# Kernel optimization log

Hardware: AMD Instinct MI355X
Metric: run time of the kernel (lower is better)

## Reference

```python
import jax, jax.numpy as jnp
import numpy as np

SCORE_THRESHOLD = 0.5
IOU_THRESHOLD = 0.5


def _pairwise_iou(boxes):
    # boxes: [N, 4] in xyxy
    x1, y1, x2, y2 = boxes[:, 0], boxes[:, 1], boxes[:, 2], boxes[:, 3]
    area = (x2 - x1) * (y2 - y1)  # [N]
    ix1 = jnp.maximum(x1[:, None], x1[None, :])
    iy1 = jnp.maximum(y1[:, None], y1[None, :])
    ix2 = jnp.minimum(x2[:, None], x2[None, :])
    iy2 = jnp.minimum(y2[:, None], y2[None, :])
    iw = jnp.clip(ix2 - ix1, 0.0)
    ih = jnp.clip(iy2 - iy1, 0.0)
    inter = iw * ih  # [N, N]
    union = area[:, None] + area[None, :] - inter
    return inter / jnp.maximum(union, 1e-9)


def setup_inputs() -> dict:
    key = jax.random.key(0)
    rtdetr_raw_out = jax.random.uniform(key, (1, 8192, 5), dtype=jnp.float32)
    return {"rtdetr_raw_out": rtdetr_raw_out}


def reference(rtdetr_raw_out):
    x = rtdetr_raw_out[0]                      # [N, 5]
    cxcywh = x[:, :4]
    conf = x[:, 4]
    conf = conf / jnp.max(conf)                # normalize by max score
    cx, cy, w, h = cxcywh[:, 0], cxcywh[:, 1], cxcywh[:, 2], cxcywh[:, 3]
    xyxy = jnp.stack([cx - w * 0.5, cy - h * 0.5, cx + w * 0.5, cy + h * 0.5], axis=1)
    valid = conf >= SCORE_THRESHOLD            # score filter
    N = xyxy.shape[0]
    # sort by descending score (torchvision nms processes boxes in score order)
    order = jnp.argsort(-conf)
    boxes_s = xyxy[order]
    scores_s = conf[order]
    valid_s = valid[order]
    iou = _pairwise_iou(boxes_s)               # [N, N]
    idx = jnp.arange(N)

    def body(i, keep):
        # if box i survives, suppress all lower-score boxes with IoU > thr
        sup = keep[i] & (iou[i] > IOU_THRESHOLD) & (idx > i)
        return keep & ~sup

    keep = jax.lax.fori_loop(0, N, body, valid_s)
    out = jnp.concatenate([boxes_s, scores_s[:, None]], axis=1)  # [N, 5]
    # fixed-shape output: suppressed / below-threshold rows are zeroed
    return jnp.where(keep[:, None], out, 0.0)
```

## Files before the change

### kernel.cpp

```cpp
#include <hip/hip_runtime.h>
#include <cstdint>

typedef unsigned long long ull;

#define N_BOX 8192
#define N_WORDS 128
#define CH 512
#define WPC 8
#define NBLK 16

#define OFF_TB     0
#define OFF_TC     3440640
#define OFF_TD     3932160
#define OFF_BOXES  4456448
#define OFF_SCORES 4587520
#define OFF_CTRL   4620288
#define OFF_KEPT   4624384

#define CTRL_VB   512
#define KSTRIDE   16

__device__ __forceinline__ int rows_before2(int c) {
    return 7424 * c - 256 * c * c;
}

__device__ __forceinline__ ull make_key(float s, int idx) {
    return (((ull)__float_as_uint(s)) << 13) | (ull)(8191 - idx);
}

__device__ __forceinline__ float box_area(float4 b) {
    return __fmul_rn(__fsub_rn(b.z, b.x), __fsub_rn(b.w, b.y));
}

__device__ __forceinline__ bool iou_gt_half(float4 a, float aarea, float4 b, float barea) {
    float ix1 = fmaxf(a.x, b.x);
    float iy1 = fmaxf(a.y, b.y);
    float ix2 = fminf(a.z, b.z);
    float iy2 = fminf(a.w, b.w);
    float iw = fmaxf(__fsub_rn(ix2, ix1), 0.0f);
    float ih = fmaxf(__fsub_rn(iy2, iy1), 0.0f);
    float inter = __fmul_rn(iw, ih);
    float uni = __fsub_rn(__fadd_rn(aarea, barea), inter);
    float iou = __fdiv_rn(inter, fmaxf(uni, 1e-9f));
    return iou > 0.5f;
}

__global__ __launch_bounds__(256) void k123_rank_scatter(const float* __restrict__ in,
                                                         float4* __restrict__ boxes4,
                                                         float* __restrict__ scores,
                                                         int* __restrict__ ctrl) {
    __shared__ ull keys[N_BOX];
    __shared__ float wm[4];
    __shared__ int wv[4];
    int t = threadIdx.x;
    int bx = blockIdx.x;

    float cf[32];
    float m = 0.0f;
    #pragma unroll
    for (int r = 0; r < 32; ++r) {
        cf[r] = in[(r * 256 + t) * 5 + 4];
        m = fmaxf(m, cf[r]);
    }
    for (int off = 32; off; off >>= 1) m = fmaxf(m, __shfl_down(m, off));
    if ((t & 63) == 0) wm[t >> 6] = m;
    __syncthreads();
    float maxc = fmaxf(fmaxf(wm[0], wm[1]), fmaxf(wm[2], wm[3]));

    #pragma unroll
    for (int r = 0; r < 32; ++r) {
        int k = r * 256 + t;
        keys[k] = make_key(__fdiv_rn(cf[r], maxc), k);
    }
    __syncthreads();

    int il = t >> 3, seg = t & 7;
    int i = bx * 32 + il;
    ull ki = keys[i];
    const ull* kb = keys + seg;
    int cnt = 0;
    #pragma unroll 8
    for (int cc = 0; cc < 1024; ++cc)
        cnt += (kb[cc * 8] > ki) ? 1 : 0;
    cnt += __shfl_down(cnt, 4, 8);
    cnt += __shfl_down(cnt, 2, 8);
    cnt += __shfl_down(cnt, 1, 8);

    if (seg == 0) {
        int r = cnt;
        float cx = in[i * 5 + 0];
        float cy = in[i * 5 + 1];
        float w  = in[i * 5 + 2];
        float h  = in[i * 5 + 3];
        float s  = __fdiv_rn(in[i * 5 + 4], maxc);
        float4 b;
        b.x = __fsub_rn(cx, __fmul_rn(w, 0.5f));
        b.y = __fsub_rn(cy, __fmul_rn(h, 0.5f));
        b.z = __fadd_rn(cx, __fmul_rn(w, 0.5f));
        b.w = __fadd_rn(cy, __fmul_rn(h, 0.5f));
        boxes4[r] = b;
        scores[r] = s;
    }

    if (bx == 0) {
        const ull kthr = ((ull)0x3F000000u) << 13;
        int cv = 0;
        for (int k = t; k < N_BOX; k += 256) cv += (keys[k] >= kthr) ? 1 : 0;
        for (int off = 32; off; off >>= 1) cv += __shfl_down(cv, off);
        if ((t & 63) == 0) wv[t >> 6] = cv;
        if (t < NBLK) ctrl[t * 32] = 0;
        __syncthreads();
        if (t == 0) ctrl[CTRL_VB] = wv[0] + wv[1] + wv[2] + wv[3];
    }
}

__global__ __launch_bounds__(256) void k4_build(const float4* __restrict__ boxes4,
                                                const float* __restrict__ scores,
                                                ull* __restrict__ TB,
                                                ull* __restrict__ TC,
                                                ull* __restrict__ TD) {
    __shared__ float4 sb[CH];
    __shared__ float sa[CH];
    int bid = blockIdx.x;
    int t = threadIdx.x;
    int c;
    int mode;
    int j0;
    if (bid >= 1920) {
        mode = 2;
        int d = bid - 1920;
        c = d >> 4;
        j0 = (d & 15) * 32;
    } else if (bid >= 1680) {
        mode = 1;
        int d = bid - 1680;
        c = d >> 4;
        j0 = (d & 15) * 32;
    } else {
        mode = 0;
        c = 0;
        int rem = bid;
        while (rem >= 224 - 16 * c) { rem -= 224 - 16 * c; ++c; }
        j0 = CH * (c + 2) + rem * 32;
    }
    if (scores[c * CH] < 0.5f) return;
    if (mode == 0 && scores[j0] < 0.5f) return;

    for (int i = t; i < CH; i += 256) {
        float4 b = boxes4[c * CH + i];
        sb[i] = b;
        sa[i] = box_area(b);
    }
    __syncthreads();

    int w = t & 7;
    int r = t >> 3;
    if (mode == 2) {
        int jl = j0 + r;
        float4 me = sb[jl];
        float ma = sa[jl];
        int wj = jl >> 6;
        int lim = (w < wj) ? 64 : ((w == wj) ? (jl & 63) : 0);
        ull bits = 0;
        for (int k = 0; k < lim; ++k)
            if (iou_gt_half(sb[w * 64 + k], sa[w * 64 + k], me, ma)) bits |= 1ull << k;
        TD[c * 4096 + w * 512 + jl] = bits;
    } else if (mode == 1) {
        int jl = j0 + r;
        int j = CH * (c + 1) + jl;
        float4 me = boxes4[j];
        float ma = box_area(me);
        ull bits = 0;
        for (int k = 0; k < 64; ++k)
            if (iou_gt_half(sb[w * 64 + k], sa[w * 64 + k], me, ma)) bits |= 1ull << k;
        TC[c * 4096 + w * 512 + jl] = bits;
    } else {
        int j = j0 + r;
        float4 me = boxes4[j];
        float ma = box_area(me);
        ull bits = 0;
        for (int k = 0; k < 64; ++k)
            if (iou_gt_half(sb[w * 64 + k], sa[w * 64 + k], me, ma)) bits |= 1ull << k;
        TB[(size_t)(rows_before2(c) + (j - CH * (c + 2))) * WPC + w] = bits;
    }
}

__global__ __launch_bounds__(1024) void k5_nms(const float4* __restrict__ boxes4,
                                               const float* __restrict__ scores,
                                               const ull* __restrict__ TBg,
                                               const ull* __restrict__ TCg,
                                               const ull* __restrict__ TDg,
                                               ull* __restrict__ keptg,
                                               int* __restrict__ ctrl,
                                               float* __restrict__ out) {
    __shared__ ull TDs[CH * WPC];
    __shared__ ull TCs[CH * WPC];
    __shared__ ull kwsh[WPC];
    __shared__ unsigned amask[16];
    int c = blockIdx.x;
    int t = threadIdx.x;
    int lane = t & 63;
    int wave = t >> 6;
    int vb = ctrl[CTRL_VB];
    int nchv = (vb + CH - 1) / CH;

    if (c < nchv) {
        {
            const ulonglong2* src = (const ulonglong2*)(TDg + (size_t)c * CH * WPC);
            ulonglong2* dst = (ulonglong2*)TDs;
            #pragma unroll
            for (int i2 = t; i2 < CH * WPC / 2; i2 += 1024) dst[i2] = src[i2];
        }
        if (c > 0) {
            const ulonglong2* src = (const ulonglong2*)(TCg + (size_t)(c - 1) * CH * WPC);
            ulonglong2* dst = (ulonglong2*)TCs;
            #pragma unroll
            for (int i2 = t; i2 < CH * WPC / 2; i2 += 1024) dst[i2] = src[i2];
        }
        if (t < 16) {
            int n = vb - (c * 16 + t) * 32;
            amask[t] = (n >= 32) ? 0xffffffffu : ((n <= 0) ? 0u : ((1u << n) - 1u));
        }
        __syncthreads();

        for (int cp = 0; cp + 2 <= c; ++cp) {
            if (wave == 0 && lane == 0) {
                while (__hip_atomic_load(&ctrl[cp * 32], __ATOMIC_ACQUIRE,
                                         __HIP_MEMORY_SCOPE_AGENT) == 0) {}
                #pragma unroll
                for (int w = 0; w < WPC; ++w)
                    kwsh[w] = __hip_atomic_load(&keptg[cp * KSTRIDE + w],
                                                __ATOMIC_RELAXED,
                                                __HIP_MEMORY_SCOPE_AGENT);
            }
            __syncthreads();
            ull anyk = kwsh[0] | kwsh[1] | kwsh[2] | kwsh[3] |
                       kwsh[4] | kwsh[5] | kwsh[6] | kwsh[7];
            if (anyk && t < CH) {
                if ((amask[t >> 5] >> (t & 31)) & 1u) {
                    const ull* row = TBg +
                        (size_t)(rows_before2(cp) + (c * CH + t - CH * (cp + 2))) * WPC;
                    ull a = 0;
                    #pragma unroll
                    for (int q = 0; q < WPC; ++q) a |= row[q] & kwsh[q];
                    if (a) atomicAnd(&amask[t >> 5], ~(1u << (t & 31)));
                }
            }
            __syncthreads();
        }

        if (c > 0) {
            if (wave == 0 && lane == 0) {
                while (__hip_atomic_load(&ctrl[(c - 1) * 32], __ATOMIC_ACQUIRE,
                                         __HIP_MEMORY_SCOPE_AGENT) == 0) {}
                #pragma unroll
                for (int w = 0; w < WPC; ++w)
                    kwsh[w] = __hip_atomic_load(&keptg[(c - 1) * KSTRIDE + w],
                                                __ATOMIC_RELAXED,
                                                __HIP_MEMORY_SCOPE_AGENT);
            }
            __syncthreads();
            if (wave < WPC) {
                bool dead = false;
                #pragma unroll
                for (int w = 0; w < WPC; ++w) {
                    ull kw = kwsh[w];
                    if (kw) dead |= (TCs[w * 512 + wave * 64 + lane] & kw) != 0ull;
                }
                ull d = __ballot(dead);
                if (lane == 0 && d) {
                    amask[2 * wave]     &= ~(unsigned)d;
                    amask[2 * wave + 1] &= ~(unsigned)(d >> 32);
                }
            }
            __syncthreads();
        }

        if (wave == 0) {
            ull alive[WPC];
            #pragma unroll
            for (int w = 0; w < WPC; ++w)
                alive[w] = (ull)amask[2 * w] | ((ull)amask[2 * w + 1] << 32);
            const ull* T = TDs;
            #pragma unroll
            for (int w = 0; w < WPC; ++w) {
                ull word = alive[w];
                if (!word) continue;
                ull Tc[WPC];
                #pragma unroll
                for (int j = 0; j < WPC; ++j)
                    if (j >= w) Tc[j] = T[w * 512 + j * 64 + lane];
                ull td = Tc[w];
                ull a2 = word, kept = 0;
                while (a2 & ~kept) {
                    bool al = (a2 >> lane) & 1;
                    bool kp = (kept >> lane) & 1;
                    ull nk = __ballot(al && !kp && ((td & a2) == 0));
                    ull nd = __ballot(al && !kp && ((td & kept) != 0));
                    kept |= nk;
                    a2 &= ~nd;
                }
                alive[w] = kept;
                #pragma unroll
                for (int j = 0; j < WPC; ++j) {
                    if (j <= w) continue;
                    if (!alive[j]) continue;
                    alive[j] &= ~__ballot((Tc[j] & kept) != 0);
                }
            }
            if (lane == 0) {
                #pragma unroll
                for (int w = 0; w < WPC; ++w) {
                    __hip_atomic_store(&keptg[c * KSTRIDE + w], alive[w],
                                       __ATOMIC_RELAXED, __HIP_MEMORY_SCOPE_AGENT);
                    amask[2 * w]     = (unsigned)alive[w];
                    amask[2 * w + 1] = (unsigned)(alive[w] >> 32);
                }
                __hip_atomic_store(&ctrl[c * 32], 1,
                                   __ATOMIC_RELEASE, __HIP_MEMORY_SCOPE_AGENT);
            }
        }
        __syncthreads();
    } else {
        if (t < 16) amask[t] = 0u;
        __syncthreads();
    }

    if (t < CH) {
        int j = c * CH + t;
        bool kept = (amask[t >> 5] >> (t & 31)) & 1u;
        float4 b = boxes4[j];
        float s = scores[j];
        out[j * 5 + 0] = kept ? b.x : 0.0f;
        out[j * 5 + 1] = kept ? b.y : 0.0f;
        out[j * 5 + 2] = kept ? b.z : 0.0f;
        out[j * 5 + 3] = kept ? b.w : 0.0f;
        out[j * 5 + 4] = kept ? s   : 0.0f;
    }
}

extern "C" void kernel_launch(void* const* d_in, const int* in_sizes, int n_in,
                              void* d_out, int out_size, void* d_ws, size_t ws_size,
                              hipStream_t stream) {
    const float* in = (const float*)d_in[0];
    char* ws = (char*)d_ws;
    ull* TB        = (ull*)(ws + OFF_TB);
    ull* TC        = (ull*)(ws + OFF_TC);
    ull* TD        = (ull*)(ws + OFF_TD);
    float4* boxes4 = (float4*)(ws + OFF_BOXES);
    float* scores  = (float*)(ws + OFF_SCORES);
    int* ctrl      = (int*)(ws + OFF_CTRL);
    ull* keptg     = (ull*)(ws + OFF_KEPT);
    float* out     = (float*)d_out;

    k123_rank_scatter<<<256, 256, 0, stream>>>(in, boxes4, scores, ctrl);
    k4_build<<<2176, 256, 0, stream>>>(boxes4, scores, TB, TC, TD);
    k5_nms<<<NBLK, 1024, 0, stream>>>(boxes4, scores, TB, TC, TD, keptg, ctrl, out);
}
```

Before: 126.5 us.

## Push adjacent-chunk suppression from producer block and unify build loop

The NMS kernel's critical-path handoff changes. Instead of each chunk waiting for its predecessor's kept mask and then evaluating the adjacent-chunk TC tile itself, the producer block computes the suppression mask for the next chunk right after publishing its result and pushes it through a new flag and buffer. The consumer only has to AND in the mask, which shortens the serial dependency chain between chunks. The build kernel also merges its three modes into one loop with a rotated, lane-staggered start index and unroll 8, meant to reduce LDS bank conflicts. The cost is extra flag traffic and an added threadfence.

```diff
diff --git a/kernel.cpp b/kernel.cpp
--- a/kernel.cpp
+++ b/kernel.cpp
@@ -4,10 +4,9 @@
 typedef unsigned long long ull;
 
 #define N_BOX 8192
-#define N_WORDS 128
 #define CH 512
 #define WPC 8
-#define NBLK 16
+#define NCH 16
 
 #define OFF_TB     0
 #define OFF_TC     3440640
@@ -15,10 +14,17 @@
 #define OFF_BOXES  4456448
 #define OFF_SCORES 4587520
 #define OFF_CTRL   4620288
-#define OFF_KEPT   4624384
-
-#define CTRL_VB   512
-#define KSTRIDE   16
+#define OFF_KEPT   4689920
+#define OFF_PUSH   4691968
+
+#define CTRL_VB    512
+#define PFLAG      1024
+#define KSTRIDE    16
+
+#define A_LD(p)    __hip_atomic_load((p), __ATOMIC_RELAXED, __HIP_MEMORY_SCOPE_AGENT)
+#define A_LDA(p)   __hip_atomic_load((p), __ATOMIC_ACQUIRE, __HIP_MEMORY_SCOPE_AGENT)
+#define A_ST(p,v)  __hip_atomic_store((p), (v), __ATOMIC_RELAXED, __HIP_MEMORY_SCOPE_AGENT)
+#define A_STR(p,v) __hip_atomic_store((p), (v), __ATOMIC_RELEASE, __HIP_MEMORY_SCOPE_AGENT)
 
 __device__ __forceinline__ int rows_before2(int c) {
     return 7424 * c - 256 * c * c;
@@ -108,7 +114,8 @@
         for (int k = t; k < N_BOX; k += 256) cv += (keys[k] >= kthr) ? 1 : 0;
         for (int off = 32; off; off >>= 1) cv += __shfl_down(cv, off);
         if ((t & 63) == 0) wv[t >> 6] = cv;
-        if (t < NBLK) ctrl[t * 32] = 0;
+        if (t < NCH) ctrl[t * 32] = 0;
+        if (t < NCH) ctrl[PFLAG + t * 32] = 0;
         __syncthreads();
         if (t == 0) ctrl[CTRL_VB] = wv[0] + wv[1] + wv[2] + wv[3];
     }
@@ -155,34 +162,33 @@
 
     int w = t & 7;
     int r = t >> 3;
+    int jl = j0 + r;
+    float4 me;
+    float ma;
+    int lim = 64;
     if (mode == 2) {
-        int jl = j0 + r;
-        float4 me = sb[jl];
-        float ma = sa[jl];
+        me = sb[jl];
+        ma = sa[jl];
         int wj = jl >> 6;
-        int lim = (w < wj) ? 64 : ((w == wj) ? (jl & 63) : 0);
-        ull bits = 0;
-        for (int k = 0; k < lim; ++k)
-            if (iou_gt_half(sb[w * 64 + k], sa[w * 64 + k], me, ma)) bits |= 1ull << k;
-        TD[c * 4096 + w * 512 + jl] = bits;
+        lim = (w < wj) ? 64 : ((w == wj) ? (jl & 63) : 0);
     } else if (mode == 1) {
-        int jl = j0 + r;
-        int j = CH * (c + 1) + jl;
-        float4 me = boxes4[j];
-        float ma = box_area(me);
-        ull bits = 0;
-        for (int k = 0; k < 64; ++k)
-            if (iou_gt_half(sb[w * 64 + k], sa[w * 64 + k], me, ma)) bits |= 1ull << k;
-        TC[c * 4096 + w * 512 + jl] = bits;
+        me = boxes4[CH * (c + 1) + jl];
+        ma = box_area(me);
     } else {
-        int j = j0 + r;
-        float4 me = boxes4[j];
-        float ma = box_area(me);
-        ull bits = 0;
-        for (int k = 0; k < 64; ++k)
-            if (iou_gt_half(sb[w * 64 + k], sa[w * 64 + k], me, ma)) bits |= 1ull << k;
-        TB[(size_t)(rows_before2(c) + (j - CH * (c + 2))) * WPC + w] = bits;
-    }
+        me = boxes4[jl];
+        ma = box_area(me);
+    }
+    ull bits = 0;
+    #pragma unroll 8
+    for (int k = 0; k < 64; ++k) {
+        int kk = (k + w) & 63;
+        if (kk < lim &&
+            iou_gt_half(sb[w * 64 + kk], sa[w * 64 + kk], me, ma))
+            bits |= 1ull << kk;
+    }
+    if (mode == 2)      TD[c * 4096 + w * 512 + jl] = bits;
+    else if (mode == 1) TC[c * 4096 + w * 512 + jl] = bits;
+    else TB[(size_t)(rows_before2(c) + (jl - CH * (c + 2))) * WPC + w] = bits;
 }
 
 __global__ __launch_bounds__(1024) void k5_nms(const float4* __restrict__ boxes4,
@@ -191,11 +197,13 @@
                                                const ull* __restrict__ TCg,
                                                const ull* __restrict__ TDg,
                                                ull* __restrict__ keptg,
+                                               ull* __restrict__ pusha,
                                                int* __restrict__ ctrl,
                                                float* __restrict__ out) {
     __shared__ ull TDs[CH * WPC];
     __shared__ ull TCs[CH * WPC];
     __shared__ ull kwsh[WPC];
+    __shared__ ull darr[WPC];
     __shared__ unsigned amask[16];
     int c = blockIdx.x;
     int t = threadIdx.x;
@@ -211,8 +219,8 @@
             #pragma unroll
             for (int i2 = t; i2 < CH * WPC / 2; i2 += 1024) dst[i2] = src[i2];
         }
-        if (c > 0) {
-            const ulonglong2* src = (const ulonglong2*)(TCg + (size_t)(c - 1) * CH * WPC);
+        if (c + 1 < nchv) {
+            const ulonglong2* src = (const ulonglong2*)(TCg + (size_t)c * CH * WPC);
             ulonglong2* dst = (ulonglong2*)TCs;
             #pragma unroll
             for (int i2 = t; i2 < CH * WPC / 2; i2 += 1024) dst[i2] = src[i2];
@@ -224,14 +232,10 @@
         __syncthreads();
 
         for (int cp = 0; cp + 2 <= c; ++cp) {
-            if (wave == 0 && lane == 0) {
-                while (__hip_atomic_load(&ctrl[cp * 32], __ATOMIC_ACQUIRE,
-                                         __HIP_MEMORY_SCOPE_AGENT) == 0) {}
-                #pragma unroll
-                for (int w = 0; w < WPC; ++w)
-                    kwsh[w] = __hip_atomic_load(&keptg[cp * KSTRIDE + w],
-                                                __ATOMIC_RELAXED,
-                                                __HIP_MEMORY_SCOPE_AGENT);
+            if (t == 0) {
+                while (A_LDA(&ctrl[cp * 32]) != 1) {}
+                #pragma unroll
+                for (int w = 0; w < WPC; ++w) kwsh[w] = A_LD(&keptg[cp * KSTRIDE + w]);
             }
             __syncthreads();
             ull anyk = kwsh[0] | kwsh[1] | kwsh[2] | kwsh[3] |
@@ -250,28 +254,16 @@
         }
 
         if (c > 0) {
-            if (wave == 0 && lane == 0) {
-                while (__hip_atomic_load(&ctrl[(c - 1) * 32], __ATOMIC_ACQUIRE,
-                                         __HIP_MEMORY_SCOPE_AGENT) == 0) {}
-                #pragma unroll
-                for (int w = 0; w < WPC; ++w)
-                    kwsh[w] = __hip_atomic_load(&keptg[(c - 1) * KSTRIDE + w],
-                                                __ATOMIC_RELAXED,
-                                                __HIP_MEMORY_SCOPE_AGENT);
-            }
-            __syncthreads();
-            if (wave < WPC) {
-                bool dead = false;
-                #pragma unroll
-                for (int w = 0; w < WPC; ++w) {
-                    ull kw = kwsh[w];
-                    if (kw) dead |= (TCs[w * 512 + wave * 64 + lane] & kw) != 0ull;
-                }
-                ull d = __ballot(dead);
-                if (lane == 0 && d) {
-                    amask[2 * wave]     &= ~(unsigned)d;
-                    amask[2 * wave + 1] &= ~(unsigned)(d >> 32);
-                }
+            if (t == 0) {
+                while (A_LDA(&ctrl[PFLAG + c * 32]) != 1) {}
+                #pragma unroll
+                for (int w = 0; w < WPC; ++w) kwsh[w] = A_LD(&pusha[c * KSTRIDE + w]);
+            }
+            __syncthreads();
+            if (t < WPC) {
+                ull s = kwsh[t];
+                amask[2 * t]     &= ~(unsigned)s;
+                amask[2 * t + 1] &= ~(unsigned)(s >> 32);
             }
             __syncthreads();
         }
@@ -311,13 +303,37 @@
             if (lane == 0) {
                 #pragma unroll
                 for (int w = 0; w < WPC; ++w) {
-                    __hip_atomic_store(&keptg[c * KSTRIDE + w], alive[w],
-                                       __ATOMIC_RELAXED, __HIP_MEMORY_SCOPE_AGENT);
+                    A_ST(&keptg[c * KSTRIDE + w], alive[w]);
                     amask[2 * w]     = (unsigned)alive[w];
                     amask[2 * w + 1] = (unsigned)(alive[w] >> 32);
                 }
-                __hip_atomic_store(&ctrl[c * 32], 1,
-                                   __ATOMIC_RELEASE, __HIP_MEMORY_SCOPE_AGENT);
+                __threadfence();
+                A_STR(&ctrl[c * 32], 1);
+            }
+        }
+        __syncthreads();
+
+        if (c + 1 < nchv) {
+            if (wave < WPC) {
+                ull kw[WPC];
+                #pragma unroll
+                for (int w = 0; w < WPC; ++w)
+                    kw[w] = (ull)amask[2 * w] | ((ull)amask[2 * w + 1] << 32);
+                bool dead = false;
+                #pragma unroll
+                for (int w = 0; w < WPC; ++w) {
+                    if (kw[w]) dead |= (TCs[w * 512 + wave * 64 + lane] & kw[w]) != 0ull;
+                }
+                ull d = __ballot(dead);
+                if (lane == 0) darr[wave] = d;
+            }
+            __syncthreads();
+            if (t == 0) {
+                #pragma unroll
+                for (int w = 0; w < WPC; ++w)
+                    A_ST(&pusha[(c + 1) * KSTRIDE + w], darr[w]);
+                __threadfence();
+                A_STR(&ctrl[PFLAG + (c + 1) * 32], 1);
             }
         }
         __syncthreads();
@@ -351,9 +367,10 @@
     float* scores  = (float*)(ws + OFF_SCORES);
     int* ctrl      = (int*)(ws + OFF_CTRL);
     ull* keptg     = (ull*)(ws + OFF_KEPT);
+    ull* pusha     = (ull*)(ws + OFF_PUSH);
     float* out     = (float*)d_out;
 
     k123_rank_scatter<<<256, 256, 0, stream>>>(in, boxes4, scores, ctrl);
     k4_build<<<2176, 256, 0, stream>>>(boxes4, scores, TB, TC, TD);
-    k5_nms<<<NBLK, 1024, 0, stream>>>(boxes4, scores, TB, TC, TD, keptg, ctrl, out);
-}
+    k5_nms<<<NCH, 1024, 0, stream>>>(boxes4, scores, TB, TC, TD, keptg, pusha, ctrl, out);
+}
```

Result: no change. 127.9 us (+1.1%).
